# Kernel tuning notes

Measured on AMD Instinct MI355X. Metric: run time of the kernel, lower is better.

Reference implementation:

```python
import jax, jax.numpy as jnp
import numpy as np

IMG = 224  # hardcoded image resolution in the original module


def setup_inputs() -> dict:
    key = jax.random.key(0)
    ks = jax.random.split(key, 6)
    b, v, n, m = 16, 8, 8192, 1024
    pc = jax.random.normal(ks[0], (b, n, 3), jnp.float32)
    # binary silhouette masks (0/1 floats), ~half zeros so many outliers exist
    mask = (jax.random.uniform(ks[1], (b, v, IMG, IMG)) < 0.5).astype(jnp.float32)
    bounds = jax.random.uniform(ks[2], (b, v, m, 2), jnp.float32) * IMG
    inv_param = jax.random.normal(ks[3], (b, v, 4, 4), jnp.float32)
    proj_fine = jax.random.uniform(ks[4], (b, v, n, 2), jnp.float32) * IMG
    proj_finez = jax.random.uniform(ks[5], (b, v, n), jnp.float32) + 0.5
    return {"pc": pc, "mask": mask, "bounds": bounds, "inv_param": inv_param,
            "proj_fine": proj_fine, "proj_finez": proj_finez, "view_id": 3}


def reference(pc, mask, bounds, inv_param, proj_fine, proj_finez, view_id):
    b = pc.shape[0]
    # --- out_distance (only view_id affects the returned pc) ---
    pxy = proj_fine[:, view_id]                                  # (b, n, 2)
    pxy = jnp.stack([pxy[..., 0], IMG - pxy[..., 1]], axis=-1)   # flip y
    pxy_i = jnp.round(pxy).astype(jnp.int32)                     # round().long()
    # ZeroPad2d(1) then index with clamp(idx+1, 0, 225)
    mv = jnp.pad(mask[:, view_id], ((0, 0), (1, 1), (1, 1)))     # (b, 226, 226)
    xi = jnp.clip(pxy_i[..., 1] + 1, 0, IMG + 1)
    yi = jnp.clip(pxy_i[..., 0] + 1, 0, IMG + 1)
    bidx = jnp.arange(b)[:, None]
    out_mask = mv[bidx, xi, yi] == 0                             # (b, n) outliers
    # K=1 KNN of (rounded) outlier pixels against boundary points, both /224
    o = pxy_i.astype(bounds.dtype) / IMG                         # (b, n, 2)
    bd = bounds[:, view_id] / IMG                                # (b, m, 2)
    d2 = ((o * o).sum(-1)[:, :, None]
          + (bd * bd).sum(-1)[:, None, :]
          - 2.0 * jnp.einsum('bnd,bmd->bnm', o, bd))             # (b, n, m)
    nn_idx = jnp.argmin(d2, axis=-1)                             # (b, n)
    # n_bound * 224 == the original boundary point, gather directly
    n_bound = jnp.take_along_axis(bounds[:, view_id], nn_idx[:, :, None], axis=1)
    # --- move_out: back-project nearest boundary point, scatter into pc ---
    z = proj_finez[:, view_id][..., None]                        # (b, n, 1)
    hom = jnp.concatenate([n_bound * z, z, jnp.ones_like(z)], axis=-1)  # (b,n,4)
    back = jnp.einsum('bnk,bkl->bnl', hom, inv_param[:, view_id])[..., :3]
    return jnp.where(out_mask[..., None], back, pc)
```

## Files before the change

kernel.cpp:

```cpp
#include <hip/hip_runtime.h>
#include <math.h>

constexpr int IMG = 224;
constexpr int Bb  = 16;
constexpr int Vv  = 8;
constexpr int Nn  = 8192;
constexpr int Mm  = 1024;
constexpr int G   = 32;
constexpr float Hh = 1.0f / 32.0f;

__global__ __launch_bounds__(256) void calib_kernel(
    const float* __restrict__ pc,
    const float* __restrict__ mask,
    const float* __restrict__ bounds,
    const float* __restrict__ inv_param,
    const float* __restrict__ proj_fine,
    const float* __restrict__ proj_finez,
    const int*   __restrict__ view_p,
    float*       __restrict__ out)
{
    const int view = *view_p;
    const int b = blockIdx.y;
    const int t = threadIdx.x;
    const int lane = t & 63;
    const int w = t >> 6;

    __shared__ float4 s_e[Mm];
    __shared__ int s_start[1025];
    __shared__ int s_cnt[1024];
    __shared__ int s_wtot[4];
    __shared__ unsigned int s_qpk[256];
    __shared__ float s_qz[256];
    __shared__ int s_qcount;

    const int ipt = blockIdx.x * 256 + t;
    const size_t pf = (size_t)(b * Vv + view) * Nn + ipt;
    float2 pxy = reinterpret_cast<const float2*>(proj_fine)[pf];
    float z    = proj_finez[pf];
    const size_t ob = ((size_t)b * Nn + ipt) * 3;
    float pc0 = pc[ob], pc1 = pc[ob + 1], pc2 = pc[ob + 2];

    if (t == 0) s_qcount = 0;
    #pragma unroll
    for (int u = 0; u < 4; ++u) s_cnt[t + 256 * u] = 0;
    __syncthreads();

    const float* bnd = bounds + (size_t)(b * Vv + view) * Mm * 2;
    float bdx[4], bdy[4];
    int cell[4];
    #pragma unroll
    for (int u = 0; u < 4; ++u) {
        int j = t + 256 * u;
        float2 bxy = reinterpret_cast<const float2*>(bnd)[j];
        bdx[u] = bxy.x / (float)IMG;
        bdy[u] = bxy.y / (float)IMG;
        int cx = min(G - 1, max(0, (int)(bdx[u] * (float)G)));
        int cy = min(G - 1, max(0, (int)(bdy[u] * (float)G)));
        cell[u] = cy * G + cx;
        atomicAdd(&s_cnt[cell[u]], 1);
    }

    int i0 = (int)rintf(pxy.x);
    int i1 = (int)rintf((float)IMG - pxy.y);
    int xi = min(max(i1 + 1, 0), IMG + 1);
    int yi = min(max(i0 + 1, 0), IMG + 1);
    float mval = 0.0f;
    if (xi >= 1 && xi <= IMG && yi >= 1 && yi <= IMG)
        mval = mask[((size_t)(b * Vv + view) * IMG + (xi - 1)) * IMG + (yi - 1)];
    __syncthreads();

    int c0 = s_cnt[4 * t], c1 = s_cnt[4 * t + 1];
    int c2 = s_cnt[4 * t + 2], c3 = s_cnt[4 * t + 3];
    int psum = c0 + c1 + c2 + c3;
    int incl = psum;
    #pragma unroll
    for (int off = 1; off < 64; off <<= 1) {
        int v = __shfl_up(incl, off);
        if (lane >= off) incl += v;
    }
    if (lane == 63) s_wtot[w] = incl;
    __syncthreads();
    int basew = 0;
    for (int ww = 0; ww < w; ++ww) basew += s_wtot[ww];
    int base = basew + incl - psum;
    s_start[4 * t] = base; s_start[4 * t + 1] = base + c0;
    s_start[4 * t + 2] = base + c0 + c1; s_start[4 * t + 3] = base + c0 + c1 + c2;
    if (t == 0) s_start[1024] = Mm;
    s_cnt[4 * t] = base; s_cnt[4 * t + 1] = base + c0;
    s_cnt[4 * t + 2] = base + c0 + c1; s_cnt[4 * t + 3] = base + c0 + c1 + c2;
    __syncthreads();

    #pragma unroll
    for (int u = 0; u < 4; ++u) {
        int j = t + 256 * u;
        int pos = atomicAdd(&s_cnt[cell[u]], 1);
        float nrm = __fadd_rn(__fmul_rn(bdx[u], bdx[u]), __fmul_rn(bdy[u], bdy[u]));
        s_e[pos] = make_float4(bdx[u], bdy[u], nrm, __int_as_float(j));
    }

    const bool use_back = (mval == 0.0f);
    if (use_back) {
        int pos = atomicAdd(&s_qcount, 1);
        s_qpk[pos] = (unsigned int)t | ((unsigned int)i0 << 8)
                   | ((unsigned int)i1 << 16);
        s_qz[pos] = z;
    } else {
        out[ob]     = pc0;
        out[ob + 1] = pc1;
        out[ob + 2] = pc2;
    }
    __syncthreads();

    const int qn = s_qcount;
    if (t >= qn) return;

    unsigned int pk = s_qpk[t];
    int p  = (int)(pk & 0xFF);
    int q0 = (int)((pk >> 8) & 0xFF);
    int q1 = (int)((pk >> 16) & 0xFF);
    float zq = s_qz[t];

    float ox = (float)q0 / (float)IMG;
    float oy = (float)q1 / (float)IMG;
    float o2 = __fadd_rn(__fmul_rn(ox, ox), __fmul_rn(oy, oy));
    float n2ox = __fmul_rn(-2.0f, ox);
    float n2oy = __fmul_rn(-2.0f, oy);

    int cx = min(G - 1, max(0, (int)(ox * (float)G)));
    int cy = min(G - 1, max(0, (int)(oy * (float)G)));

    float best = INFINITY;
    int   bj   = 0;

    int x0 = max(cx - 2, 0), x1 = min(cx + 2, G - 1);
    int bases[5], offs[5];
    int T = 0;
    #pragma unroll
    for (int r = 0; r < 5; ++r) {
        int yy = cy - 2 + r;
        int bb = 0, LL = 0;
        if (yy >= 0 && yy < G) {
            int rowb = yy * G;
            int e0 = s_start[rowb + x0];
            int e1 = s_start[rowb + x1 + 1];
            bb = e0; LL = e1 - e0;
        }
        bases[r] = bb; offs[r] = T; T += LL;
    }
    for (int u = 0; u < T; ++u) {
        int base2 = bases[0], off2 = offs[0];
        #pragma unroll
        for (int r = 1; r < 5; ++r) {
            bool in = (u >= offs[r]);
            base2 = in ? bases[r] : base2;
            off2  = in ? offs[r]  : off2;
        }
        float4 cd = s_e[base2 + (u - off2)];
        float dn = __fadd_rn(__fmul_rn(n2ox, cd.x), __fmul_rn(n2oy, cd.y));
        float d2 = __fadd_rn(__fadd_rn(o2, cd.z), dn);
        int   j  = __float_as_int(cd.w);
        bool better = (d2 < best) || (d2 == best && j < bj);
        best = better ? d2 : best;
        bj   = better ? j  : bj;
    }

    if (!(best < 4.0f * Hh * Hh - 1e-5f)) {
        for (int r = 3; r <= G; ++r) {
            float lim = (float)(r - 1) * Hh;
            if (best < lim * lim - 1e-5f) break;
            int rx0 = max(0, cx - r), rx1 = min(G - 1, cx + r);
            int ry0 = max(0, cy - r), ry1 = min(G - 1, cy + r);
            for (int yy = ry0; yy <= ry1; ++yy) {
                bool yedge = (yy == cy - r) || (yy == cy + r);
                for (int xx = rx0; xx <= rx1; ++xx) {
                    if (!yedge && xx != cx - r && xx != cx + r) continue;
                    int c = yy * G + xx;
                    int e0 = s_start[c], e1 = s_start[c + 1];
                    for (int e = e0; e < e1; ++e) {
                        float4 cd = s_e[e];
                        float dn = __fadd_rn(__fmul_rn(n2ox, cd.x), __fmul_rn(n2oy, cd.y));
                        float d2 = __fadd_rn(__fadd_rn(o2, cd.z), dn);
                        int   j  = __float_as_int(cd.w);
                        bool better = (d2 < best) || (d2 == best && j < bj);
                        best = better ? d2 : best;
                        bj   = better ? j  : bj;
                    }
                }
            }
        }
    }

    float nbx = bnd[2 * bj];
    float nby = bnd[2 * bj + 1];
    const float* ip = inv_param + (size_t)(b * Vv + view) * 16;
    float h0 = nbx * zq, h1 = nby * zq;
    float r0 = h0 * ip[0] + h1 * ip[4] + zq * ip[8]  + ip[12];
    float r1 = h0 * ip[1] + h1 * ip[5] + zq * ip[9]  + ip[13];
    float r2 = h0 * ip[2] + h1 * ip[6] + zq * ip[10] + ip[14];

    const size_t obq = ((size_t)b * Nn + blockIdx.x * 256 + p) * 3;
    out[obq]     = r0;
    out[obq + 1] = r1;
    out[obq + 2] = r2;
}

extern "C" void kernel_launch(void* const* d_in, const int* in_sizes, int n_in,
                              void* d_out, int out_size, void* d_ws, size_t ws_size,
                              hipStream_t stream) {
    const float* pc         = (const float*)d_in[0];
    const float* mask       = (const float*)d_in[1];
    const float* bounds     = (const float*)d_in[2];
    const float* inv_param  = (const float*)d_in[3];
    const float* proj_fine  = (const float*)d_in[4];
    const float* proj_finez = (const float*)d_in[5];
    const int*   view_p     = (const int*)d_in[6];
    float* out = (float*)d_out;

    dim3 grid(Nn / 256, Bb);
    calib_kernel<<<grid, 256, 0, stream>>>(pc, mask, bounds, inv_param,
                                           proj_fine, proj_finez, view_p, out);
}
```

Before: 19.07 us.

## Halve points per block to double grid and hoist boundary loads

Each 256-thread block now handles 128 query points instead of 256, doubling the grid to 64x16 blocks. All 256 threads still build the shared boundary grid, but only half load points and do the KNN search. Boundary loads are also issued at kernel start so they overlap the point and mask loads. This trades twice the redundant per-block grid construction for more blocks and parallelism across CUs, and shorter per-block tails in the serial search loop.

```diff
diff --git a/kernel.cpp b/kernel.cpp
--- a/kernel.cpp
+++ b/kernel.cpp
@@ -29,44 +29,58 @@
     __shared__ int s_start[1025];
     __shared__ int s_cnt[1024];
     __shared__ int s_wtot[4];
-    __shared__ unsigned int s_qpk[256];
-    __shared__ float s_qz[256];
+    __shared__ unsigned int s_qpk[128];
+    __shared__ float s_qz[128];
     __shared__ int s_qcount;
 
-    const int ipt = blockIdx.x * 256 + t;
+    const float* bnd = bounds + (size_t)(b * Vv + view) * Mm * 2;
+    float2 bxy0 = reinterpret_cast<const float2*>(bnd)[t];
+    float2 bxy1 = reinterpret_cast<const float2*>(bnd)[t + 256];
+    float2 bxy2 = reinterpret_cast<const float2*>(bnd)[t + 512];
+    float2 bxy3 = reinterpret_cast<const float2*>(bnd)[t + 768];
+
+    const bool haspt = (t < 128);
+    const int ipt = blockIdx.x * 128 + (t & 127);
     const size_t pf = (size_t)(b * Vv + view) * Nn + ipt;
-    float2 pxy = reinterpret_cast<const float2*>(proj_fine)[pf];
-    float z    = proj_finez[pf];
+    float2 pxy = make_float2(0.f, 0.f);
+    float z = 0.f, pc0 = 0.f, pc1 = 0.f, pc2 = 0.f;
     const size_t ob = ((size_t)b * Nn + ipt) * 3;
-    float pc0 = pc[ob], pc1 = pc[ob + 1], pc2 = pc[ob + 2];
+    if (haspt) {
+        pxy = reinterpret_cast<const float2*>(proj_fine)[pf];
+        z   = proj_finez[pf];
+        pc0 = pc[ob]; pc1 = pc[ob + 1]; pc2 = pc[ob + 2];
+    }
 
     if (t == 0) s_qcount = 0;
     #pragma unroll
     for (int u = 0; u < 4; ++u) s_cnt[t + 256 * u] = 0;
-    __syncthreads();
-
-    const float* bnd = bounds + (size_t)(b * Vv + view) * Mm * 2;
+
+    int i0 = 0, i1 = 0;
+    float mval = 0.0f;
+    if (haspt) {
+        i0 = (int)rintf(pxy.x);
+        i1 = (int)rintf((float)IMG - pxy.y);
+        int xi = min(max(i1 + 1, 0), IMG + 1);
+        int yi = min(max(i0 + 1, 0), IMG + 1);
+        if (xi >= 1 && xi <= IMG && yi >= 1 && yi <= IMG)
+            mval = mask[((size_t)(b * Vv + view) * IMG + (xi - 1)) * IMG + (yi - 1)];
+    }
+    __syncthreads();
+
     float bdx[4], bdy[4];
     int cell[4];
-    #pragma unroll
-    for (int u = 0; u < 4; ++u) {
-        int j = t + 256 * u;
-        float2 bxy = reinterpret_cast<const float2*>(bnd)[j];
-        bdx[u] = bxy.x / (float)IMG;
-        bdy[u] = bxy.y / (float)IMG;
-        int cx = min(G - 1, max(0, (int)(bdx[u] * (float)G)));
-        int cy = min(G - 1, max(0, (int)(bdy[u] * (float)G)));
-        cell[u] = cy * G + cx;
-        atomicAdd(&s_cnt[cell[u]], 1);
-    }
-
-    int i0 = (int)rintf(pxy.x);
-    int i1 = (int)rintf((float)IMG - pxy.y);
-    int xi = min(max(i1 + 1, 0), IMG + 1);
-    int yi = min(max(i0 + 1, 0), IMG + 1);
-    float mval = 0.0f;
-    if (xi >= 1 && xi <= IMG && yi >= 1 && yi <= IMG)
-        mval = mask[((size_t)(b * Vv + view) * IMG + (xi - 1)) * IMG + (yi - 1)];
+    {
+        float2 ba[4] = {bxy0, bxy1, bxy2, bxy3};
+        #pragma unroll
+        for (int u = 0; u < 4; ++u) {
+            bdx[u] = ba[u].x / (float)IMG;
+            bdy[u] = ba[u].y / (float)IMG;
+            int cx = min(G - 1, max(0, (int)(bdx[u] * (float)G)));
+            int cy = min(G - 1, max(0, (int)(bdy[u] * (float)G)));
+            cell[u] = cy * G + cx;
+            atomicAdd(&s_cnt[cell[u]], 1);
+        }
+    }
     __syncthreads();
 
     int c0 = s_cnt[4 * t], c1 = s_cnt[4 * t + 1];
@@ -98,16 +112,17 @@
         s_e[pos] = make_float4(bdx[u], bdy[u], nrm, __int_as_float(j));
     }
 
-    const bool use_back = (mval == 0.0f);
-    if (use_back) {
-        int pos = atomicAdd(&s_qcount, 1);
-        s_qpk[pos] = (unsigned int)t | ((unsigned int)i0 << 8)
-                   | ((unsigned int)i1 << 16);
-        s_qz[pos] = z;
-    } else {
-        out[ob]     = pc0;
-        out[ob + 1] = pc1;
-        out[ob + 2] = pc2;
+    if (haspt) {
+        if (mval == 0.0f) {
+            int pos = atomicAdd(&s_qcount, 1);
+            s_qpk[pos] = (unsigned int)(t & 127) | ((unsigned int)i0 << 8)
+                       | ((unsigned int)i1 << 16);
+            s_qz[pos] = z;
+        } else {
+            out[ob]     = pc0;
+            out[ob + 1] = pc1;
+            out[ob + 2] = pc2;
+        }
     }
     __syncthreads();
 
@@ -198,7 +213,7 @@
     float r1 = h0 * ip[1] + h1 * ip[5] + zq * ip[9]  + ip[13];
     float r2 = h0 * ip[2] + h1 * ip[6] + zq * ip[10] + ip[14];
 
-    const size_t obq = ((size_t)b * Nn + blockIdx.x * 256 + p) * 3;
+    const size_t obq = ((size_t)b * Nn + blockIdx.x * 128 + p) * 3;
     out[obq]     = r0;
     out[obq + 1] = r1;
     out[obq + 2] = r2;
@@ -216,7 +231,7 @@
     const int*   view_p     = (const int*)d_in[6];
     float* out = (float*)d_out;
 
-    dim3 grid(Nn / 256, Bb);
+    dim3 grid(Nn / 128, Bb);
     calib_kernel<<<grid, 256, 0, stream>>>(pc, mask, bounds, inv_param,
                                            proj_fine, proj_finez, view_p, out);
 }
```

Result: slower. 20.33 us (+6.6%).
